# Kernel optimization log

Measured on AMD Instinct MI355X. Metric: run time of the kernel, lower is better.

## Reference

```python
import jax, jax.numpy as jnp
import numpy as np

N = 100000          # nodes
E = 1000000         # edges (before self-loops)
NFEAT = 512
NHID = 32
HEADS = 8
NCLASS = 40
SLOPE = 0.2         # PyG GATConv negative_slope


def gat_conv(x, W, a_src, a_dst, bias, src, dst, heads, out_c, concat):
    """PyG-style GATConv (eval mode, self-loops already appended to src/dst)."""
    n = x.shape[0]
    h = (x @ W).reshape(n, heads, out_c)                      # [N, H, C]
    e_src = jnp.sum(h * a_src, axis=-1)                       # [N, H]
    e_dst = jnp.sum(h * a_dst, axis=-1)                       # [N, H]
    e = jax.nn.leaky_relu(e_src[src] + e_dst[dst], SLOPE)     # [E, H]
    m = jax.ops.segment_max(e, dst, num_segments=n)           # per-dst max
    ex = jnp.exp(e - m[dst])
    den = jax.ops.segment_sum(ex, dst, num_segments=n)        # [N, H]
    alpha = ex / den[dst]                                     # softmax over in-edges
    out = jax.ops.segment_sum(alpha[:, :, None] * h[src], dst, num_segments=n)
    out = out.reshape(n, heads * out_c) if concat else out.mean(axis=1)
    return out + bias


def setup_inputs() -> dict:
    key = jax.random.key(0)
    ks = jax.random.split(key, 10)
    x = jax.random.normal(ks[0], (N, NFEAT), dtype=jnp.float32)
    edge_index = jax.random.randint(ks[1], (2, E), 0, N, dtype=jnp.int64)
    s1 = 1.0 / np.sqrt(NFEAT)
    s2 = 1.0 / np.sqrt(HEADS * NHID)
    return {
        "x": x,
        "edge_index": edge_index,
        "W1": jax.random.normal(ks[2], (NFEAT, HEADS * NHID), dtype=jnp.float32) * s1,
        "a_src1": jax.random.normal(ks[3], (HEADS, NHID), dtype=jnp.float32) * s2,
        "a_dst1": jax.random.normal(ks[4], (HEADS, NHID), dtype=jnp.float32) * s2,
        "b1": jnp.zeros((HEADS * NHID,), dtype=jnp.float32),
        "W2": jax.random.normal(ks[5], (HEADS * NHID, NCLASS), dtype=jnp.float32) * s2,
        "a_src2": jax.random.normal(ks[6], (1, NCLASS), dtype=jnp.float32) * 0.1,
        "a_dst2": jax.random.normal(ks[7], (1, NCLASS), dtype=jnp.float32) * 0.1,
        "b2": jnp.zeros((NCLASS,), dtype=jnp.float32),
    }


def reference(x, edge_index, W1, a_src1, a_dst1, b1, W2, a_src2, a_dst2, b2):
    loop = jnp.arange(N, dtype=edge_index.dtype)
    src = jnp.concatenate([edge_index[0], loop])
    dst = jnp.concatenate([edge_index[1], loop])
    # layer 1: nfeat -> heads*nhid (concat), ELU  (dropout is identity in eval)
    h1 = jax.nn.elu(gat_conv(x, W1, a_src1, a_dst1, b1, src, dst, HEADS, NHID, True))
    # layer 2: heads*nhid -> nclass, single head, concat=False
    logits = gat_conv(h1, W2, a_src2, a_dst2, b2, src, dst, 1, NCLASS, False)
    return jax.nn.log_softmax(logits, axis=1), h1
```

## Files before the change

kernel.cpp:

```cpp
#include <hip/hip_runtime.h>

#define NN 100000
#define EE 1000000
#define NFEAT 512
#define NHID 32
#define HEADS 8
#define F1 256
#define NCLASS 40
#define SLOPE 0.2f
#define NB1 98

typedef __bf16 bf16x8 __attribute__((ext_vector_type(8)));
typedef float f32x4 __attribute__((ext_vector_type(4)));

union BF8 { unsigned short s[8]; bf16x8 v; uint4 u; };

__device__ __forceinline__ float bf2f(unsigned short u) {
    return __uint_as_float(((unsigned)u) << 16);
}
__device__ __forceinline__ unsigned short f2bf(float f) {
    unsigned x = __float_as_uint(f);
    unsigned r = (x + 0x7fffu + ((x >> 16) & 1u)) >> 16;
    return (unsigned short)r;
}
__device__ __forceinline__ float lrelu(float x) { return x > 0.f ? x : SLOPE * x; }

__global__ void detect_i64(const int* __restrict__ ei, int* __restrict__ flag) {
    int i = blockIdx.x * 256 + threadIdx.x;
    if (i < 4096) {
        if (ei[2 * i + 1] != 0) atomicOr(flag, 1);
    }
}
__global__ void canon_edges(const int* __restrict__ ei, const int* __restrict__ flag,
                            int* __restrict__ srcC, int* __restrict__ dstC,
                            int* __restrict__ deg) {
    int e = blockIdx.x * 256 + threadIdx.x;
    if (e >= EE) return;
    int s, d;
    if (*flag) {
        s = ei[e];
        d = ei[EE + e];
    } else {
        s = ei[2 * e];
        d = ei[2 * EE + 2 * e];
    }
    srcC[e] = s;
    dstC[e] = d;
    atomicAdd(deg + d, 1);
}

__global__ void scan1(const int* __restrict__ deg, int* __restrict__ bsum) {
    __shared__ int s[256];
    int b = blockIdx.x, t = threadIdx.x;
    int base = b * 1024 + t * 4, sum = 0;
    #pragma unroll
    for (int j = 0; j < 4; j++) { int i = base + j; sum += (i < NN) ? deg[i] : 0; }
    s[t] = sum; __syncthreads();
    for (int off = 128; off > 0; off >>= 1) {
        if (t < off) s[t] += s[t + off];
        __syncthreads();
    }
    if (t == 0) bsum[b] = s[0];
}
__global__ void scan2(int* __restrict__ bsum, int* __restrict__ row_ptr) {
    if (threadIdx.x == 0 && blockIdx.x == 0) {
        int acc = 0;
        for (int i = 0; i < NB1; i++) { int v = bsum[i]; bsum[i] = acc; acc += v; }
        row_ptr[NN] = EE;
    }
}
__global__ void scan3(const int* __restrict__ deg, const int* __restrict__ bsum,
                      int* __restrict__ row_ptr, int* __restrict__ pos) {
    __shared__ int ts[256];
    int b = blockIdx.x, t = threadIdx.x;
    int base = b * 1024 + t * 4;
    int v[4], sum = 0;
    #pragma unroll
    for (int j = 0; j < 4; j++) { int i = base + j; v[j] = (i < NN) ? deg[i] : 0; sum += v[j]; }
    ts[t] = sum; __syncthreads();
    for (int off = 1; off < 256; off <<= 1) {
        int add = (t >= off) ? ts[t - off] : 0;
        __syncthreads();
        ts[t] += add;
        __syncthreads();
    }
    int prefix = bsum[b] + ts[t] - sum;
    #pragma unroll
    for (int j = 0; j < 4; j++) {
        int i = base + j;
        if (i < NN) { row_ptr[i] = prefix; pos[i] = prefix; prefix += v[j]; }
    }
}
__global__ void fill_csr(const int* __restrict__ srcC, const int* __restrict__ dstC,
                         int* __restrict__ pos, int* __restrict__ eadj) {
    int e = blockIdx.x * 256 + threadIdx.x;
    if (e >= EE) return;
    int idx = atomicAdd(pos + dstC[e], 1);
    eadj[idx] = srcC[e];
}

__global__ void prep_w1(const float* __restrict__ w1, unsigned short* __restrict__ w1tb) {
    int t = blockIdx.x * 256 + threadIdx.x;
    if (t < NFEAT * F1) {
        int k = t / F1, n = t % F1;
        w1tb[n * NFEAT + k] = f2bf(w1[t]);
    }
}

__device__ __forceinline__ void stage_b(const unsigned short* __restrict__ w1tb,
                                        unsigned short* bs, int kk, int tid) {
    #pragma unroll
    for (int j = 0; j < 4; j++) {
        int c = j * 256 + tid;
        int n = c >> 2, part = c & 3;
        const unsigned short* src = w1tb + n * NFEAT + kk * 32 + part * 8;
        unsigned short* dst = bs + c * 8;
        __builtin_amdgcn_global_load_lds(
            (const __attribute__((address_space(1))) unsigned int*)src,
            (__attribute__((address_space(3))) unsigned int*)dst, 16, 0, 0);
    }
}

__global__ __launch_bounds__(256) void gemm1_kernel(
    const float* __restrict__ x, const unsigned short* __restrict__ w1tb,
    unsigned short* __restrict__ hb) {
    __shared__ unsigned short Bs[2][256 * 32];
    int tid = threadIdx.x;
    int wave = tid >> 6, lane = tid & 63;
    int quad = lane >> 4, r = lane & 15;
    int mBase = blockIdx.x * 64 + wave * 16;
    long arow = mBase + r; if (arow > NN - 1) arow = NN - 1;
    const float* aptr = x + arow * NFEAT + quad * 8;

    stage_b(w1tb, Bs[0], 0, tid);

    f32x4 acc[16];
    #pragma unroll
    for (int t = 0; t < 16; t++) acc[t] = {0.f, 0.f, 0.f, 0.f};

    for (int kk = 0; kk < 16; kk++) {
        float4 fa0 = *(const float4*)(aptr + kk * 32);
        float4 fa1 = *(const float4*)(aptr + kk * 32 + 4);
        float fa[8] = {fa0.x, fa0.y, fa0.z, fa0.w, fa1.x, fa1.y, fa1.z, fa1.w};
        BF8 ah;
        #pragma unroll
        for (int j = 0; j < 8; j++) ah.s[j] = f2bf(fa[j]);
        __syncthreads();
        if (kk + 1 < 16) stage_b(w1tb, Bs[(kk + 1) & 1], kk + 1, tid);
        const unsigned short* bsc = Bs[kk & 1];
        #pragma unroll
        for (int t = 0; t < 16; t++) {
            BF8 vb;
            vb.u = *(const uint4*)(bsc + (t * 16 + r) * 32 + quad * 8);
            acc[t] = __builtin_amdgcn_mfma_f32_16x16x32_bf16(ah.v, vb.v, acc[t], 0, 0, 0);
        }
    }
    #pragma unroll
    for (int i = 0; i < 4; i++) {
        int m = mBase + quad * 4 + i;
        if (m < NN) {
            unsigned short* hp = hb + (long)m * F1 + r;
            #pragma unroll
            for (int t = 0; t < 16; t++) hp[t * 16] = f2bf(acc[t][i]);
        }
    }
}

__global__ __launch_bounds__(256) void escore1_kernel(
    const unsigned short* __restrict__ hb, const float* __restrict__ a_src,
    const float* __restrict__ a_dst, float* __restrict__ es, float* __restrict__ ed) {
    __shared__ float As[F1], Ad[F1];
    int tid = threadIdx.x;
    As[tid] = a_src[tid];
    Ad[tid] = a_dst[tid];
    __syncthreads();
    int t = blockIdx.x * 256 + tid;
    if (t >= NN * HEADS) return;
    int n = t >> 3, hd = t & 7;
    const uint4* hp = (const uint4*)(hb + (long)n * F1 + hd * NHID);
    float s = 0.f, d = 0.f;
    #pragma unroll
    for (int q = 0; q < 4; q++) {
        uint4 u = hp[q];
        unsigned vv[4] = {u.x, u.y, u.z, u.w};
        #pragma unroll
        for (int w = 0; w < 4; w++) {
            float lo = bf2f((unsigned short)(vv[w] & 0xffffu));
            float hi = bf2f((unsigned short)(vv[w] >> 16));
            int c = q * 8 + w * 2;
            s += lo * As[hd * NHID + c] + hi * As[hd * NHID + c + 1];
            d += lo * Ad[hd * NHID + c] + hi * Ad[hd * NHID + c + 1];
        }
    }
    es[t] = s; ed[t] = d;
}

__global__ __launch_bounds__(256) void gat1_fused(
    const int* __restrict__ row_ptr, const int* __restrict__ eadj,
    const float* __restrict__ es, const float* __restrict__ ed,
    const unsigned short* __restrict__ hb, const float* __restrict__ b1,
    float* __restrict__ h1o) {
    int wave = threadIdx.x >> 6, lane = threadIdx.x & 63;
    int d = blockIdx.x * 4 + wave;
    if (d >= NN) return;
    int eslot = lane >> 3, hd8 = lane & 7, hdo = lane >> 3;
    float edv = ed[d * 8 + hd8];
    int beg = row_ptr[d], end = row_ptr[d + 1];

    float mself = lrelu(es[d * 8 + hd8] + edv);
    float m = mself;
    float den = (eslot == 0) ? 1.f : 0.f;
    ushort4 hv = ((const ushort4*)(hb + (long)d * F1))[lane];
    float ax = bf2f(hv.x), ay = bf2f(hv.y);
    float az = bf2f(hv.z), aw = bf2f(hv.w);

    for (int i = beg; i < end; i += 8) {
        int idx = i + eslot;
        int s = (idx < end) ? eadj[idx] : 0;
        float el = lrelu(es[s * 8 + hd8] + edv);
        if (idx >= end) el = -1e30f;
        float gm = el;
        gm = fmaxf(gm, __shfl_xor(gm, 8));
        gm = fmaxf(gm, __shfl_xor(gm, 16));
        gm = fmaxf(gm, __shfl_xor(gm, 32));
        float mn = fmaxf(m, gm);
        float rsc = __expf(m - mn);
        m = mn;
        den *= rsc;
        float ro = __shfl(rsc, hdo);
        ax *= ro; ay *= ro; az *= ro; aw *= ro;

        float wj = (idx < end) ? __expf(el - m) : 0.f;
        den += wj;
        int cnt = min(8, end - i);
        if (cnt == 8) {
            #pragma unroll
            for (int j = 0; j < 8; j++) {
                float w = __shfl(wj, j * 8 + hdo);
                int sj = __shfl(s, j * 8);
                ushort4 v = ((const ushort4*)(hb + (long)sj * F1))[lane];
                ax += w * bf2f(v.x); ay += w * bf2f(v.y);
                az += w * bf2f(v.z); aw += w * bf2f(v.w);
            }
        } else {
            for (int j = 0; j < cnt; j++) {
                float w = __shfl(wj, j * 8 + hdo);
                int sj = __shfl(s, j * 8);
                ushort4 v = ((const ushort4*)(hb + (long)sj * F1))[lane];
                ax += w * bf2f(v.x); ay += w * bf2f(v.y);
                az += w * bf2f(v.z); aw += w * bf2f(v.w);
            }
        }
    }
    den += __shfl_xor(den, 8);
    den += __shfl_xor(den, 16);
    den += __shfl_xor(den, 32);
    float deno = __shfl(den, hdo);

    float4 bb = ((const float4*)b1)[lane];
    float inv = 1.f / deno;
    float rx = ax * inv + bb.x, ry = ay * inv + bb.y;
    float rz = az * inv + bb.z, rw = aw * inv + bb.w;
    rx = rx > 0.f ? rx : expm1f(rx);
    ry = ry > 0.f ? ry : expm1f(ry);
    rz = rz > 0.f ? rz : expm1f(rz);
    rw = rw > 0.f ? rw : expm1f(rw);
    float4 r = {rx, ry, rz, rw};
    ((float4*)(h1o + (long)d * F1))[lane] = r;
}

__global__ __launch_bounds__(256) void gemm2_kernel(const float* __restrict__ h1,
                                                    const float* __restrict__ w2,
                                                    float* __restrict__ h2) {
    __shared__ float4 Ws[F1 * 10];
    for (int i = threadIdx.x; i < F1 * 10; i += 256) Ws[i] = ((const float4*)w2)[i];
    __syncthreads();
    long t = (long)blockIdx.x * 256 + threadIdx.x;
    if (t >= (long)NN * 10) return;
    int n = (int)(t / 10);
    int j = (int)(t - (long)n * 10);
    const float4* hp = (const float4*)(h1 + (long)n * F1);
    float4 a = {0.f, 0.f, 0.f, 0.f};
    #pragma unroll 8
    for (int k4 = 0; k4 < 64; k4++) {
        float4 hv = hp[k4];
        float4 w0 = Ws[(k4 * 4 + 0) * 10 + j];
        float4 w1v = Ws[(k4 * 4 + 1) * 10 + j];
        float4 w2v = Ws[(k4 * 4 + 2) * 10 + j];
        float4 w3v = Ws[(k4 * 4 + 3) * 10 + j];
        a.x += hv.x * w0.x + hv.y * w1v.x + hv.z * w2v.x + hv.w * w3v.x;
        a.y += hv.x * w0.y + hv.y * w1v.y + hv.z * w2v.y + hv.w * w3v.y;
        a.z += hv.x * w0.z + hv.y * w1v.z + hv.z * w2v.z + hv.w * w3v.z;
        a.w += hv.x * w0.w + hv.y * w1v.w + hv.z * w2v.w + hv.w * w3v.w;
    }
    ((float4*)(h2 + (long)n * NCLASS))[j] = a;
}

__global__ void escore2_kernel(const float* __restrict__ h2,
                               const float* __restrict__ a_src2,
                               const float* __restrict__ a_dst2,
                               float* __restrict__ e2s, float* __restrict__ e2d) {
    __shared__ float As[NCLASS], Ad[NCLASS];
    if (threadIdx.x < NCLASS) {
        As[threadIdx.x] = a_src2[threadIdx.x];
        Ad[threadIdx.x] = a_dst2[threadIdx.x];
    }
    __syncthreads();
    int n = blockIdx.x * 256 + threadIdx.x;
    if (n >= NN) return;
    const float* hp = h2 + (long)n * NCLASS;
    float s = 0.f, d = 0.f;
    #pragma unroll
    for (int c = 0; c < NCLASS; c++) {
        float v = hp[c];
        s += v * As[c];
        d += v * Ad[c];
    }
    e2s[n] = s; e2d[n] = d;
}

__global__ __launch_bounds__(256) void gat2_logsm(
    const int* __restrict__ row_ptr, const int* __restrict__ eadj,
    const float* __restrict__ e2s, const float* __restrict__ e2d,
    const float* __restrict__ h2, const float* __restrict__ b2,
    float* __restrict__ out0) {
    int wave = threadIdx.x >> 6, lane = threadIdx.x & 63;
    int d = blockIdx.x * 4 + wave;
    if (d >= NN) return;
    int eslot = lane >> 3, c8 = lane & 7;
    float edv = e2d[d];
    int beg = row_ptr[d], end = row_ptr[d + 1];

    float mself = lrelu(e2s[d] + edv);
    float m = mself;
    float den = (eslot == 0) ? 1.f : 0.f;
    float acc[5];
    {
        const float* hp = h2 + (long)d * NCLASS + c8 * 5;
        #pragma unroll
        for (int k = 0; k < 5; k++) acc[k] = (eslot == 0) ? hp[k] : 0.f;
    }

    for (int i = beg; i < end; i += 8) {
        int idx = i + eslot;
        int s = (idx < end) ? eadj[idx] : 0;
        float el = lrelu(e2s[s] + edv);
        if (idx >= end) el = -1e30f;
        float gm = el;
        gm = fmaxf(gm, __shfl_xor(gm, 8));
        gm = fmaxf(gm, __shfl_xor(gm, 16));
        gm = fmaxf(gm, __shfl_xor(gm, 32));
        float mn = fmaxf(m, gm);
        float rsc = __expf(m - mn);
        m = mn;
        den *= rsc;
        #pragma unroll
        for (int k = 0; k < 5; k++) acc[k] *= rsc;
        float wj = (idx < end) ? __expf(el - m) : 0.f;
        den += wj;
        if (idx < end) {
            const float* hp = h2 + (long)s * NCLASS + c8 * 5;
            #pragma unroll
            for (int k = 0; k < 5; k++) acc[k] += wj * hp[k];
        }
    }
    #pragma unroll
    for (int off = 8; off <= 32; off <<= 1) {
        den += __shfl_xor(den, off);
        #pragma unroll
        for (int k = 0; k < 5; k++) acc[k] += __shfl_xor(acc[k], off);
    }
    float inv = 1.f / den;
    float v[5];
    float mx = -1e30f;
    #pragma unroll
    for (int k = 0; k < 5; k++) {
        v[k] = acc[k] * inv + b2[c8 * 5 + k];
        mx = fmaxf(mx, v[k]);
    }
    #pragma unroll
    for (int off = 1; off <= 4; off <<= 1) mx = fmaxf(mx, __shfl_xor(mx, off));
    float sm = 0.f;
    #pragma unroll
    for (int k = 0; k < 5; k++) sm += __expf(v[k] - mx);
    #pragma unroll
    for (int off = 1; off <= 4; off <<= 1) sm += __shfl_xor(sm, off);
    float ls = mx + logf(sm);
    if (eslot == 0) {
        float* op = out0 + (long)d * NCLASS + c8 * 5;
        #pragma unroll
        for (int k = 0; k < 5; k++) op[k] = v[k] - ls;
    }
}

extern "C" void kernel_launch(void* const* d_in, const int* in_sizes, int n_in,
                              void* d_out, int out_size, void* d_ws, size_t ws_size,
                              hipStream_t stream) {
    const float* x   = (const float*)d_in[0];
    const int* ei    = (const int*)d_in[1];
    const float* W1  = (const float*)d_in[2];
    const float* as1 = (const float*)d_in[3];
    const float* ad1 = (const float*)d_in[4];
    const float* b1  = (const float*)d_in[5];
    const float* W2  = (const float*)d_in[6];
    const float* as2 = (const float*)d_in[7];
    const float* ad2 = (const float*)d_in[8];
    const float* b2  = (const float*)d_in[9];

    float* out0 = (float*)d_out;
    float* h1o  = out0 + (long)NN * NCLASS;

    unsigned short* hb = (unsigned short*)d_ws;
    unsigned short* w1tb = hb + (long)NN * F1;
    float* es1  = (float*)(w1tb + F1 * NFEAT);
    float* ed1  = es1 + NN * HEADS;
    float* e2s  = ed1 + NN * HEADS;
    float* e2d  = e2s + NN;
    int* srcC   = (int*)(e2d + NN);
    int* dstC   = srcC + EE;
    int* eadj   = dstC + EE;
    int* deg    = eadj + EE;
    int* row_ptr= deg + NN;
    int* pos    = row_ptr + NN + 1;
    int* bsum   = pos + NN;
    int* flag   = bsum + NB1;
    float* h2   = (float*)d_ws;

    hipMemsetAsync(flag, 0, 4, stream);
    hipMemsetAsync(deg, 0, (size_t)NN * 4, stream);

    detect_i64<<<16, 256, 0, stream>>>(ei, flag);
    canon_edges<<<(EE + 255) / 256, 256, 0, stream>>>(ei, flag, srcC, dstC, deg);
    scan1<<<NB1, 256, 0, stream>>>(deg, bsum);
    scan2<<<1, 64, 0, stream>>>(bsum, row_ptr);
    scan3<<<NB1, 256, 0, stream>>>(deg, bsum, row_ptr, pos);
    fill_csr<<<(EE + 255) / 256, 256, 0, stream>>>(srcC, dstC, pos, eadj);

    prep_w1<<<(NFEAT * F1 + 255) / 256, 256, 0, stream>>>(W1, w1tb);
    gemm1_kernel<<<(NN + 63) / 64, 256, 0, stream>>>(x, w1tb, hb);
    escore1_kernel<<<(NN * HEADS) / 256, 256, 0, stream>>>(hb, as1, ad1, es1, ed1);
    gat1_fused<<<(NN + 3) / 4, 256, 0, stream>>>(row_ptr, eadj, es1, ed1, hb, b1, h1o);

    gemm2_kernel<<<(int)(((long)NN * 10 + 255) / 256), 256, 0, stream>>>(h1o, W2, h2);
    escore2_kernel<<<(NN + 255) / 256, 256, 0, stream>>>(h2, as2, ad2, e2s, e2d);
    gat2_logsm<<<(NN + 3) / 4, 256, 0, stream>>>(row_ptr, eadj, e2s, e2d, h2, b2, out0);
}
```

Before: 716.4 us.

## Fuse attention scores into GEMM1 epilogue and widen GAT1 gather loads

Computes the per-head source and destination attention scores inside the GEMM1 epilogue with cross-lane shuffle reductions, and removes the separate escore kernel along with its re-read of h. The GAT1 aggregation now has each half-wave handle alternate edges with 16-byte loads per lane, processing two edges per step, and combines the halves at the end. It also replaces the serial single-thread block-sum scan with a wave-shuffle scan and reads the edge index as int2 vectors. The cost is more registers and shuffles in the GEMM epilogue and a final cross-half reduction in the gather.

Result: no change. 711.5 us (-0.7%).

```diff
diff --git a/kernel.cpp b/kernel.cpp
--- a/kernel.cpp
+++ b/kernel.cpp
@@ -41,8 +41,10 @@
         s = ei[e];
         d = ei[EE + e];
     } else {
-        s = ei[2 * e];
-        d = ei[2 * EE + 2 * e];
+        int2 a = ((const int2*)ei)[e];
+        int2 b = ((const int2*)ei)[EE + e];
+        s = a.x;
+        d = b.x;
     }
     srcC[e] = s;
     dstC[e] = d;
@@ -63,11 +65,26 @@
     if (t == 0) bsum[b] = s[0];
 }
 __global__ void scan2(int* __restrict__ bsum, int* __restrict__ row_ptr) {
-    if (threadIdx.x == 0 && blockIdx.x == 0) {
-        int acc = 0;
-        for (int i = 0; i < NB1; i++) { int v = bsum[i]; bsum[i] = acc; acc += v; }
-        row_ptr[NN] = EE;
-    }
+    int lane = threadIdx.x;
+    int v0 = (lane < NB1) ? bsum[lane] : 0;
+    int v1 = (64 + lane < NB1) ? bsum[64 + lane] : 0;
+    int s0 = v0;
+    #pragma unroll
+    for (int off = 1; off < 64; off <<= 1) {
+        int t = __shfl_up(s0, off);
+        if (lane >= off) s0 += t;
+    }
+    int tot0 = __shfl(s0, 63);
+    int s1 = v1;
+    #pragma unroll
+    for (int off = 1; off < 64; off <<= 1) {
+        int t = __shfl_up(s1, off);
+        if (lane >= off) s1 += t;
+    }
+    s1 += tot0;
+    if (lane < NB1) bsum[lane] = s0 - v0;
+    if (64 + lane < NB1) bsum[64 + lane] = s1 - v1;
+    if (lane == 0) row_ptr[NN] = EE;
 }
 __global__ void scan3(const int* __restrict__ deg, const int* __restrict__ bsum,
                       int* __restrict__ row_ptr, int* __restrict__ pos) {
@@ -123,9 +140,13 @@
 
 __global__ __launch_bounds__(256) void gemm1_kernel(
     const float* __restrict__ x, const unsigned short* __restrict__ w1tb,
-    unsigned short* __restrict__ hb) {
+    const float* __restrict__ a_src, const float* __restrict__ a_dst,
+    unsigned short* __restrict__ hb, float* __restrict__ es, float* __restrict__ ed) {
     __shared__ unsigned short Bs[2][256 * 32];
+    __shared__ float As_[F1], Ad_[F1];
     int tid = threadIdx.x;
+    As_[tid] = a_src[tid];
+    Ad_[tid] = a_dst[tid];
     int wave = tid >> 6, lane = tid & 63;
     int quad = lane >> 4, r = lane & 15;
     int mBase = blockIdx.x * 64 + wave * 16;
@@ -163,36 +184,30 @@
             #pragma unroll
             for (int t = 0; t < 16; t++) hp[t * 16] = f2bf(acc[t][i]);
         }
-    }
-}
-
-__global__ __launch_bounds__(256) void escore1_kernel(
-    const unsigned short* __restrict__ hb, const float* __restrict__ a_src,
-    const float* __restrict__ a_dst, float* __restrict__ es, float* __restrict__ ed) {
-    __shared__ float As[F1], Ad[F1];
-    int tid = threadIdx.x;
-    As[tid] = a_src[tid];
-    Ad[tid] = a_dst[tid];
-    __syncthreads();
-    int t = blockIdx.x * 256 + tid;
-    if (t >= NN * HEADS) return;
-    int n = t >> 3, hd = t & 7;
-    const uint4* hp = (const uint4*)(hb + (long)n * F1 + hd * NHID);
-    float s = 0.f, d = 0.f;
-    #pragma unroll
-    for (int q = 0; q < 4; q++) {
-        uint4 u = hp[q];
-        unsigned vv[4] = {u.x, u.y, u.z, u.w};
-        #pragma unroll
-        for (int w = 0; w < 4; w++) {
-            float lo = bf2f((unsigned short)(vv[w] & 0xffffu));
-            float hi = bf2f((unsigned short)(vv[w] >> 16));
-            int c = q * 8 + w * 2;
-            s += lo * As[hd * NHID + c] + hi * As[hd * NHID + c + 1];
-            d += lo * Ad[hd * NHID + c] + hi * Ad[hd * NHID + c + 1];
-        }
-    }
-    es[t] = s; ed[t] = d;
+        float pv[16];
+        #pragma unroll
+        for (int k = 0; k < 16; k++) pv[k] = 0.f;
+        #pragma unroll
+        for (int t = 0; t < 16; t++) {
+            float hv = bf2f(f2bf(acc[t][i]));
+            int hd = t >> 1;
+            pv[hd]     += hv * As_[t * 16 + r];
+            pv[8 + hd] += hv * Ad_[t * 16 + r];
+        }
+        #pragma unroll
+        for (int b = 1; b <= 8; b <<= 1) {
+            #pragma unroll
+            for (int k = 0; k < 16; k++) pv[k] += __shfl_xor(pv[k], b);
+        }
+        if (m < NN) {
+            float v = pv[0];
+            #pragma unroll
+            for (int k = 1; k < 16; k++) v = (r == k) ? pv[k] : v;
+            int hd = r & 7;
+            if (r < 8) es[(long)m * 8 + hd] = v;
+            else       ed[(long)m * 8 + hd] = v;
+        }
+    }
 }
 
 __global__ __launch_bounds__(256) void gat1_fused(
@@ -203,16 +218,25 @@
     int wave = threadIdx.x >> 6, lane = threadIdx.x & 63;
     int d = blockIdx.x * 4 + wave;
     if (d >= NN) return;
-    int eslot = lane >> 3, hd8 = lane & 7, hdo = lane >> 3;
+    int eslot = lane >> 3, hd8 = lane & 7;
+    int half = lane >> 5, sub = lane & 31, hh = sub >> 2;
     float edv = ed[d * 8 + hd8];
     int beg = row_ptr[d], end = row_ptr[d + 1];
 
     float mself = lrelu(es[d * 8 + hd8] + edv);
     float m = mself;
     float den = (eslot == 0) ? 1.f : 0.f;
-    ushort4 hv = ((const ushort4*)(hb + (long)d * F1))[lane];
-    float ax = bf2f(hv.x), ay = bf2f(hv.y);
-    float az = bf2f(hv.z), aw = bf2f(hv.w);
+
+    float a0, a1, a2, a3, a4, a5, a6, a7;
+    if (half == 0) {
+        uint4 u = ((const uint4*)(hb + (long)d * F1))[sub];
+        a0 = bf2f((unsigned short)(u.x & 0xffffu)); a1 = bf2f((unsigned short)(u.x >> 16));
+        a2 = bf2f((unsigned short)(u.y & 0xffffu)); a3 = bf2f((unsigned short)(u.y >> 16));
+        a4 = bf2f((unsigned short)(u.z & 0xffffu)); a5 = bf2f((unsigned short)(u.z >> 16));
+        a6 = bf2f((unsigned short)(u.w & 0xffffu)); a7 = bf2f((unsigned short)(u.w >> 16));
+    } else {
+        a0 = a1 = a2 = a3 = a4 = a5 = a6 = a7 = 0.f;
+    }
 
     for (int i = beg; i < end; i += 8) {
         int idx = i + eslot;
@@ -227,46 +251,57 @@
         float rsc = __expf(m - mn);
         m = mn;
         den *= rsc;
-        float ro = __shfl(rsc, hdo);
-        ax *= ro; ay *= ro; az *= ro; aw *= ro;
-
         float wj = (idx < end) ? __expf(el - m) : 0.f;
         den += wj;
+        float ro = __shfl(rsc, hh);
+        a0 *= ro; a1 *= ro; a2 *= ro; a3 *= ro;
+        a4 *= ro; a5 *= ro; a6 *= ro; a7 *= ro;
+
         int cnt = min(8, end - i);
-        if (cnt == 8) {
-            #pragma unroll
-            for (int j = 0; j < 8; j++) {
-                float w = __shfl(wj, j * 8 + hdo);
-                int sj = __shfl(s, j * 8);
-                ushort4 v = ((const ushort4*)(hb + (long)sj * F1))[lane];
-                ax += w * bf2f(v.x); ay += w * bf2f(v.y);
-                az += w * bf2f(v.z); aw += w * bf2f(v.w);
-            }
-        } else {
-            for (int j = 0; j < cnt; j++) {
-                float w = __shfl(wj, j * 8 + hdo);
-                int sj = __shfl(s, j * 8);
-                ushort4 v = ((const ushort4*)(hb + (long)sj * F1))[lane];
-                ax += w * bf2f(v.x); ay += w * bf2f(v.y);
-                az += w * bf2f(v.z); aw += w * bf2f(v.w);
+        #pragma unroll
+        for (int jj = 0; jj < 4; jj++) {
+            int e = jj * 2 + half;
+            float w = __shfl(wj, e * 8 + hh);
+            int sj = __shfl(s, e * 8);
+            if (e < cnt) {
+                uint4 u = ((const uint4*)(hb + (long)sj * F1))[sub];
+                a0 += w * bf2f((unsigned short)(u.x & 0xffffu));
+                a1 += w * bf2f((unsigned short)(u.x >> 16));
+                a2 += w * bf2f((unsigned short)(u.y & 0xffffu));
+                a3 += w * bf2f((unsigned short)(u.y >> 16));
+                a4 += w * bf2f((unsigned short)(u.z & 0xffffu));
+                a5 += w * bf2f((unsigned short)(u.z >> 16));
+                a6 += w * bf2f((unsigned short)(u.w & 0xffffu));
+                a7 += w * bf2f((unsigned short)(u.w >> 16));
             }
         }
     }
     den += __shfl_xor(den, 8);
     den += __shfl_xor(den, 16);
     den += __shfl_xor(den, 32);
-    float deno = __shfl(den, hdo);
-
-    float4 bb = ((const float4*)b1)[lane];
-    float inv = 1.f / deno;
-    float rx = ax * inv + bb.x, ry = ay * inv + bb.y;
-    float rz = az * inv + bb.z, rw = aw * inv + bb.w;
-    rx = rx > 0.f ? rx : expm1f(rx);
-    ry = ry > 0.f ? ry : expm1f(ry);
-    rz = rz > 0.f ? rz : expm1f(rz);
-    rw = rw > 0.f ? rw : expm1f(rw);
-    float4 r = {rx, ry, rz, rw};
-    ((float4*)(h1o + (long)d * F1))[lane] = r;
+    float deno = __shfl(den, hh);
+
+    a0 += __shfl_xor(a0, 32); a1 += __shfl_xor(a1, 32);
+    a2 += __shfl_xor(a2, 32); a3 += __shfl_xor(a3, 32);
+    a4 += __shfl_xor(a4, 32); a5 += __shfl_xor(a5, 32);
+    a6 += __shfl_xor(a6, 32); a7 += __shfl_xor(a7, 32);
+
+    if (half == 0) {
+        float inv = 1.f / deno;
+        float4 blo = ((const float4*)b1)[sub * 2];
+        float4 bhi = ((const float4*)b1)[sub * 2 + 1];
+        float r0 = a0 * inv + blo.x, r1 = a1 * inv + blo.y;
+        float r2 = a2 * inv + blo.z, r3 = a3 * inv + blo.w;
+        float r4 = a4 * inv + bhi.x, r5 = a5 * inv + bhi.y;
+        float r6 = a6 * inv + bhi.z, r7 = a7 * inv + bhi.w;
+        r0 = r0 > 0.f ? r0 : expm1f(r0); r1 = r1 > 0.f ? r1 : expm1f(r1);
+        r2 = r2 > 0.f ? r2 : expm1f(r2); r3 = r3 > 0.f ? r3 : expm1f(r3);
+        r4 = r4 > 0.f ? r4 : expm1f(r4); r5 = r5 > 0.f ? r5 : expm1f(r5);
+        r6 = r6 > 0.f ? r6 : expm1f(r6); r7 = r7 > 0.f ? r7 : expm1f(r7);
+        float4 o0 = {r0, r1, r2, r3}, o1 = {r4, r5, r6, r7};
+        ((float4*)(h1o + (long)d * F1))[sub * 2] = o0;
+        ((float4*)(h1o + (long)d * F1))[sub * 2 + 1] = o1;
+    }
 }
 
 __global__ __launch_bounds__(256) void gemm2_kernel(const float* __restrict__ h1,
@@ -437,8 +472,7 @@
     fill_csr<<<(EE + 255) / 256, 256, 0, stream>>>(srcC, dstC, pos, eadj);
 
     prep_w1<<<(NFEAT * F1 + 255) / 256, 256, 0, stream>>>(W1, w1tb);
-    gemm1_kernel<<<(NN + 63) / 64, 256, 0, stream>>>(x, w1tb, hb);
-    escore1_kernel<<<(NN * HEADS) / 256, 256, 0, stream>>>(hb, as1, ad1, es1, ed1);
+    gemm1_kernel<<<(NN + 63) / 64, 256, 0, stream>>>(x, w1tb, as1, ad1, hb, es1, ed1);
     gat1_fused<<<(NN + 3) / 4, 256, 0, stream>>>(row_ptr, eadj, es1, ed1, hb, b1, h1o);
 
     gemm2_kernel<<<(int)(((long)NN * 10 + 255) / 256), 256, 0, stream>>>(h1o, W2, h2);
```
